# Performance work log

Measured on AMD Instinct MI355X. Metric: run time of the kernel, lower is better.

## Reference

```python
import jax, jax.numpy as jnp
import numpy as np

H, W, C_IN, C_OUT, N = 512, 512, 256, 256, 65536


def setup_inputs() -> dict:
    key = jax.random.key(0)
    k1, k2, k3, k4 = jax.random.split(key, 4)
    feature = jax.random.normal(k1, (1, C_IN, H, W), dtype=jnp.float32)
    weight = jax.random.normal(k2, (C_OUT, C_IN, 3, 3), dtype=jnp.float32) * 0.05
    # base sparse locations in the unpadded map; build 3x3 neighborhood indices
    # into the PADDED ([H+2, W+2]) map, exactly like F.pad + fancy indexing.
    base_h = jax.random.randint(k3, (N,), 0, H, dtype=jnp.int32)
    base_w = jax.random.randint(k4, (N,), 0, W, dtype=jnp.int32)
    dh = jnp.repeat(jnp.arange(3, dtype=jnp.int32), 3)  # [9]: 0,0,0,1,1,1,2,2,2
    dw = jnp.tile(jnp.arange(3, dtype=jnp.int32), 3)    # [9]: 0,1,2,0,1,2,...
    h_idx = base_h[None, :] + dh[:, None]  # [9, N], values in [0, H+1]
    w_idx = base_w[None, :] + dw[:, None]  # [9, N], values in [0, W+1]
    return {"feature": feature, "weight": weight, "h_idx": h_idx, "w_idx": w_idx}


def reference(feature, weight, h_idx, w_idx):
    # feature: [1, C, H, W]; weight: [Cout, C, 3, 3]; h_idx/w_idx: [9, N]
    C = feature.shape[1]
    out_ch = weight.shape[0]
    # F.pad(feature, [1,1,1,1])[0] -> [C, H+2, W+2]
    padded = jnp.pad(feature, ((0, 0), (0, 0), (1, 1), (1, 1)))[0]
    # gather 3x3 neighborhoods at sparse locations -> [C, 9, N]
    gathered = padded[:, h_idx, w_idx]
    # .view(9*C, -1): contiguous reshape gives row index c*9 + k
    g = gathered.reshape(C * 9, -1)  # [C*9, N]
    # kernel_d2s = weight.view(out, -1): row ordering c*9 + (kh*3+kw) matches
    k2d = weight.reshape(out_ch, -1)  # [Cout, C*9]
    return k2d @ g  # [Cout, N]
```

## Files before the change

### kernel.cpp

```cpp
#include <hip/hip_runtime.h>
#include <hip/hip_bf16.h>

#define HH 512
#define WW 512
#define CIN 256
#define COUT 256
#define NPTS 65536
#define PW 514
#define NPIX (PW * PW)
#define NKT 72

typedef __bf16 bf16x8 __attribute__((ext_vector_type(8)));
typedef float f32x16 __attribute__((ext_vector_type(16)));
typedef unsigned short us8 __attribute__((ext_vector_type(8)));

static __device__ __forceinline__ unsigned short f2bf(float f) {
  unsigned u = __builtin_bit_cast(unsigned, f);
  unsigned r = u + 0x7fffu + ((u >> 16) & 1u);
  return (unsigned short)(r >> 16);
}

static __device__ __forceinline__ void gload16(const void* g, void* l) {
  __builtin_amdgcn_global_load_lds(
      (const __attribute__((address_space(1))) unsigned int*)g,
      (__attribute__((address_space(3))) unsigned int*)l, 16, 0, 0);
}

__global__ __launch_bounds__(256) void prep_weight(const float* __restrict__ w,
                                                   unsigned short* __restrict__ A) {
  int i = blockIdx.x * 256 + threadIdx.x;
  int kt = i >> 13;
  int o  = i & 8191;
  int r  = o >> 5;
  int cp = (o >> 3) & 3;
  int j  = o & 7;
  int c  = cp ^ ((r >> 1) & 3);
  int k  = kt * 32 + c * 8 + j;
  int t  = k >> 8;
  int ci = k & 255;
  A[i] = f2bf(__builtin_nontemporal_load(&w[r * 2304 + ci * 9 + t]));
}

__global__ __launch_bounds__(256) void border_zero(unsigned short* __restrict__ Ft) {
  int g = blockIdx.x * 256 + threadIdx.x;
  if (g >= 2052 * 32) return;
  int p = g >> 5, c = g & 31;
  int py, px;
  if (p < 514)        { py = 0;        px = p; }
  else if (p < 1028)  { py = 513;      px = p - 514; }
  else if (p < 1540)  { py = p - 1027; px = 0; }
  else                { py = p - 1539; px = 513; }
  *(us8*)&Ft[((size_t)py * PW + px) * 256 + c * 8] = (us8){0, 0, 0, 0, 0, 0, 0, 0};
}

__global__ __launch_bounds__(256) void transpose_feat(const float* __restrict__ f,
                                                      unsigned short* __restrict__ Ft) {
  __shared__ unsigned short lds[64 * 264];
  int pix0 = blockIdx.x * 64;
  int y = pix0 >> 9, x0 = pix0 & 511;
  int tid = threadIdx.x;
  int p = tid & 63;
  int cb = tid >> 6;
  const float* src = f + pix0 + p;
  for (int c8 = 0; c8 < 8; ++c8) {
    us8 v;
#pragma unroll
    for (int j = 0; j < 8; ++j) {
      int ci = cb * 64 + c8 * 8 + j;
      v[j] = f2bf(__builtin_nontemporal_load(&src[ci * 262144]));
    }
    *(us8*)&lds[p * 264 + cb * 64 + c8 * 8] = v;
  }
  __syncthreads();
  int cic = tid & 31;
  int pr = tid >> 5;
  for (int g = 0; g < 8; ++g) {
    int p2 = pr + g * 8;
    us8 v = *(const us8*)&lds[p2 * 264 + cic * 8];
    *(us8*)&Ft[((size_t)((y + 1) * PW + x0 + 1 + p2)) * 256 + cic * 8] = v;
  }
}

__global__ __launch_bounds__(512, 2) void gemm_gather(
    const unsigned short* __restrict__ A,
    const unsigned short* __restrict__ Ft,
    const int* __restrict__ hidx,
    const int* __restrict__ widx,
    float* __restrict__ out) {
  __shared__ unsigned short lds[73728];
  unsigned short* ldsB = lds + 24576;

  int tid = threadIdx.x;
  int lane = tid & 63, wv = tid >> 6;
  int wm = wv & 1, wn = wv >> 1;
  int n0 = blockIdx.x << 8;

  int pxc = tid >> 3;
  int lcB = (tid & 7) ^ (pxc & 7);
  const unsigned short *FtP0, *FtP1, *FtP2, *FtP3;
  {
    FtP0 = Ft + (long)(hidx[n0 + pxc] * PW + widx[n0 + pxc]) * 256 + lcB * 8;
    FtP1 = Ft + (long)(hidx[n0 + 64 + pxc] * PW + widx[n0 + 64 + pxc]) * 256 + lcB * 8;
    FtP2 = Ft + (long)(hidx[n0 + 128 + pxc] * PW + widx[n0 + 128 + pxc]) * 256 + lcB * 8;
    FtP3 = Ft + (long)(hidx[n0 + 192 + pxc] * PW + widx[n0 + 192 + pxc]) * 256 + lcB * 8;
  }

#define STAGE_A(t_, ab_)                                                      \
  do {                                                                        \
    const unsigned short* g_ = A + (size_t)(t_) * 8192 + tid * 8;             \
    unsigned short* l_ = lds + (ab_) * 8192 + tid * 8;                        \
    gload16(g_, l_);                                                          \
    gload16(g_ + 4096, l_ + 4096);                                            \
  } while (0)

#define STAGE_BP(q_, bb_)                                                     \
  do {                                                                        \
    int tap_ = (q_) >> 2;                                                     \
    long off_ = (long)((tap_ / 3) * PW + (tap_ - (tap_ / 3) * 3)) * 256 +     \
                ((q_) & 3) * 64;                                              \
    unsigned short* l_ = ldsB + (bb_) * 16384 + tid * 8;                      \
    gload16(FtP0 + off_, l_);                                                 \
    gload16(FtP1 + off_, l_ + 4096);                                          \
    gload16(FtP2 + off_, l_ + 8192);                                          \
    gload16(FtP3 + off_, l_ + 12288);                                         \
  } while (0)

#define LDA(dst, ab_, kg_, mt_)                                               \
  do {                                                                        \
    int r_ = wm * 128 + (mt_) * 32 + (lane & 31);                             \
    int c_ = ((kg_) * 2 + (lane >> 5)) ^ ((r_ >> 1) & 3);                     \
    dst = *(const bf16x8*)&lds[(ab_) * 8192 + r_ * 32 + c_ * 8];              \
  } while (0)

#define LDB(dst, bb_, s_, kg_, nt_)                                           \
  do {                                                                        \
    int col_ = wn * 64 + (nt_) * 32 + (lane & 31);                            \
    int ph_ = ((s_) * 4 + (kg_) * 2 + (lane >> 5)) ^ (col_ & 7);              \
    dst = *(const bf16x8*)&ldsB[(bb_) * 16384 + col_ * 64 + ph_ * 8];         \
  } while (0)

#define MFMA8(a0, a1, a2, a3, b0, b1)                                         \
  do {                                                                        \
    __builtin_amdgcn_s_setprio(1);                                            \
    acc[0][0] = __builtin_amdgcn_mfma_f32_32x32x16_bf16(a0, b0, acc[0][0], 0, 0, 0); \
    acc[0][1] = __builtin_amdgcn_mfma_f32_32x32x16_bf16(a0, b1, acc[0][1], 0, 0, 0); \
    acc[1][0] = __builtin_amdgcn_mfma_f32_32x32x16_bf16(a1, b0, acc[1][0], 0, 0, 0); \
    acc[1][1] = __builtin_amdgcn_mfma_f32_32x32x16_bf16(a1, b1, acc[1][1], 0, 0, 0); \
    acc[2][0] = __builtin_amdgcn_mfma_f32_32x32x16_bf16(a2, b0, acc[2][0], 0, 0, 0); \
    acc[2][1] = __builtin_amdgcn_mfma_f32_32x32x16_bf16(a2, b1, acc[2][1], 0, 0, 0); \
    acc[3][0] = __builtin_amdgcn_mfma_f32_32x32x16_bf16(a3, b0, acc[3][0], 0, 0, 0); \
    acc[3][1] = __builtin_amdgcn_mfma_f32_32x32x16_bf16(a3, b1, acc[3][1], 0, 0, 0); \
    __builtin_amdgcn_s_setprio(0);                                            \
  } while (0)

#define HEAD()                                                                \
  do {                                                                        \
    asm volatile("s_waitcnt lgkmcnt(0)" ::: "memory");                        \
    asm volatile("s_waitcnt vmcnt(6)" ::: "memory");                          \
    __builtin_amdgcn_s_barrier();                                             \
    __builtin_amdgcn_sched_barrier(0);                                        \
  } while (0)

#define TILE(ab_, bb_, s_, ...)                                               \
  do {                                                                        \
    HEAD();                                                                   \
    bf16x8 xa0, xa1, xa2, xa3, xb0, xb1, ya0, ya1, ya2, ya3, yb0, yb1;        \
    LDA(xa0, ab_, 0, 0); LDA(xa1, ab_, 0, 1); LDA(xa2, ab_, 0, 2);            \
    LDA(xa3, ab_, 0, 3); LDB(xb0, bb_, s_, 0, 0); LDB(xb1, bb_, s_, 0, 1);    \
    __VA_ARGS__;                                                              \
    LDA(ya0, ab_, 1, 0); LDA(ya1, ab_, 1, 1); LDA(ya2, ab_, 1, 2);            \
    LDA(ya3, ab_, 1, 3); LDB(yb0, bb_, s_, 1, 0); LDB(yb1, bb_, s_, 1, 1);    \
    MFMA8(xa0, xa1, xa2, xa3, xb0, xb1);                                      \
    MFMA8(ya0, ya1, ya2, ya3, yb0, yb1);                                      \
  } while (0)

  f32x16 acc[4][2];
#pragma unroll
  for (int mt = 0; mt < 4; ++mt)
#pragma unroll
    for (int nt = 0; nt < 2; ++nt)
      acc[mt][nt] = (f32x16)(0.f);

  STAGE_BP(0, 0);
  STAGE_A(0, 0);
  STAGE_A(1, 1);
  STAGE_BP(1, 1);

  for (int P3 = 0; P3 < 12; ++P3) {
#pragma unroll
    for (int v = 0; v < 3; ++v) {
      int q = P3 * 3 + v;
      int t = 2 * q;
      TILE((2 * v) % 3, v, 0,
           STAGE_A((t + 2 < NKT ? t + 2 : NKT - 1), (2 * v + 2) % 3);
           STAGE_BP((q + 2 < 36 ? q + 2 : 35), (v + 2) % 3));
      TILE((2 * v + 1) % 3, v, 1,
           STAGE_A((t + 3 < NKT ? t + 3 : NKT - 1), (2 * v) % 3));
    }
  }

#undef STAGE_A
#undef STAGE_BP
#undef LDA
#undef LDB
#undef MFMA8
#undef HEAD
#undef TILE

  int colb = n0 + wn * 64 + (lane & 31);
  int rb = wm * 128 + ((lane >> 5) << 2);
#pragma unroll
  for (int mt = 0; mt < 4; ++mt)
#pragma unroll
    for (int nt = 0; nt < 2; ++nt)
#pragma unroll
      for (int r = 0; r < 16; ++r) {
        int row = rb + mt * 32 + (r & 3) + ((r >> 2) << 3);
        __builtin_nontemporal_store(acc[mt][nt][r],
                                    &out[(size_t)row * NPTS + colb + nt * 32]);
      }
}

__global__ __launch_bounds__(256) void naive_conv(const float* __restrict__ f,
                                                  const float* __restrict__ w,
                                                  const int* __restrict__ hi,
                                                  const int* __restrict__ wi,
                                                  float* __restrict__ out) {
  int idx = blockIdx.x * 256 + threadIdx.x;
  int n = idx & (NPTS - 1);
  int co = idx >> 16;
  int bh = hi[n] - 1;
  int bw = wi[n] - 1;
  float acc = 0.f;
  for (int ci = 0; ci < CIN; ++ci) {
    const float* fc = f + (size_t)ci * 262144;
    const float* wc = w + (size_t)co * 2304 + ci * 9;
#pragma unroll
    for (int t = 0; t < 9; ++t) {
      int y = bh + t / 3, x = bw + t % 3;
      float v = (y >= 0 && y < 512 && x >= 0 && x < 512) ? fc[y * 512 + x] : 0.f;
      acc += wc[t] * v;
    }
  }
  out[(size_t)co * NPTS + n] = acc;
}

extern "C" void kernel_launch(void* const* d_in, const int* in_sizes, int n_in,
                              void* d_out, int out_size, void* d_ws, size_t ws_size,
                              hipStream_t stream) {
  const float* feature = (const float*)d_in[0];
  const float* weight  = (const float*)d_in[1];
  const int* hidx      = (const int*)d_in[2];
  const int* widx      = (const int*)d_in[3];
  float* out           = (float*)d_out;

  const size_t FT_OFF = 2ull * 1024 * 1024;
  const size_t FT_BYTES = (size_t)NPIX * 256 * 2;
  const size_t NEED = FT_OFF + FT_BYTES;

  if (ws_size >= NEED) {
    unsigned short* Abf = (unsigned short*)d_ws;
    unsigned short* Ft = (unsigned short*)((char*)d_ws + FT_OFF);
    prep_weight<<<(NKT * 8192) / 256, 256, 0, stream>>>(weight, Abf);
    border_zero<<<(2052 * 32 + 255) / 256, 256, 0, stream>>>(Ft);
    transpose_feat<<<262144 / 64, 256, 0, stream>>>(feature, Ft);
    gemm_gather<<<NPTS / 256, 512, 0, stream>>>(Abf, Ft, hidx, widx, out);
  } else {
    naive_conv<<<(COUT * NPTS) / 256, 256, 0, stream>>>(feature, weight, hidx, widx, out);
  }
}
```

Measured before the change: 159.8 us.

## Split each K-tile into two barrier-separated MFMA phases interleaving LDS reads with staging

Restructures the inner tile so each k-tile runs in two halves, each with its own LDS fragment loads, a barrier plus lgkmcnt wait, and eight MFMAs over half the M-tiles. Global-to-LDS staging for A and B is split between the two halves, and the vmcnt wait and barrier move to the end of the tile, with an extra wait before the loop. The aim is a ping-pong style schedule where waves overlap LDS reads and async loads with MFMA work at lower register pressure. The cost is more barriers per tile and reloading A fragments in the second phase.

```diff
diff --git a/kernel.cpp b/kernel.cpp
--- a/kernel.cpp
+++ b/kernel.cpp
@@ -120,7 +120,7 @@
                 ((q_) & 3) * 64;                                              \
     unsigned short* l_ = ldsB + (bb_) * 16384 + tid * 8;                      \
     gload16(FtP0 + off_, l_);                                                 \
-    gload16(FtP1 + off_, l_ + 4096);                                          \
+    gload16(FtP1 + off_, l_ + 4096);                                         \
     gload16(FtP2 + off_, l_ + 8192);                                          \
     gload16(FtP3 + off_, l_ + 12288);                                         \
   } while (0)
@@ -139,39 +139,43 @@
     dst = *(const bf16x8*)&ldsB[(bb_) * 16384 + col_ * 64 + ph_ * 8];         \
   } while (0)
 
-#define MFMA8(a0, a1, a2, a3, b0, b1)                                         \
-  do {                                                                        \
+#define MF(x_, y_, z_) __builtin_amdgcn_mfma_f32_32x32x16_bf16(x_, y_, z_, 0, 0, 0)
+
+#define SYNC_LGKM()                                                           \
+  do {                                                                        \
+    __builtin_amdgcn_s_barrier();                                             \
+    asm volatile("s_waitcnt lgkmcnt(0)" ::: "memory");                        \
+    __builtin_amdgcn_sched_barrier(0);                                        \
+  } while (0)
+
+#define TILE(ab_, bb_, s_, STGA, STGB)                                        \
+  do {                                                                        \
+    bf16x8 a0, a1, a2, a3, b0, b1, b2, b3;                                    \
+    LDA(a0, ab_, 0, 0); LDA(a1, ab_, 0, 1);                                   \
+    LDA(a2, ab_, 1, 0); LDA(a3, ab_, 1, 1);                                   \
+    LDB(b0, bb_, s_, 0, 0); LDB(b1, bb_, s_, 0, 1);                           \
+    LDB(b2, bb_, s_, 1, 0); LDB(b3, bb_, s_, 1, 1);                           \
+    STGA;                                                                     \
+    SYNC_LGKM();                                                              \
     __builtin_amdgcn_s_setprio(1);                                            \
-    acc[0][0] = __builtin_amdgcn_mfma_f32_32x32x16_bf16(a0, b0, acc[0][0], 0, 0, 0); \
-    acc[0][1] = __builtin_amdgcn_mfma_f32_32x32x16_bf16(a0, b1, acc[0][1], 0, 0, 0); \
-    acc[1][0] = __builtin_amdgcn_mfma_f32_32x32x16_bf16(a1, b0, acc[1][0], 0, 0, 0); \
-    acc[1][1] = __builtin_amdgcn_mfma_f32_32x32x16_bf16(a1, b1, acc[1][1], 0, 0, 0); \
-    acc[2][0] = __builtin_amdgcn_mfma_f32_32x32x16_bf16(a2, b0, acc[2][0], 0, 0, 0); \
-    acc[2][1] = __builtin_amdgcn_mfma_f32_32x32x16_bf16(a2, b1, acc[2][1], 0, 0, 0); \
-    acc[3][0] = __builtin_amdgcn_mfma_f32_32x32x16_bf16(a3, b0, acc[3][0], 0, 0, 0); \
-    acc[3][1] = __builtin_amdgcn_mfma_f32_32x32x16_bf16(a3, b1, acc[3][1], 0, 0, 0); \
+    acc[0][0] = MF(a0, b0, acc[0][0]); acc[0][1] = MF(a0, b1, acc[0][1]);     \
+    acc[1][0] = MF(a1, b0, acc[1][0]); acc[1][1] = MF(a1, b1, acc[1][1]);     \
+    acc[0][0] = MF(a2, b2, acc[0][0]); acc[0][1] = MF(a2, b3, acc[0][1]);     \
+    acc[1][0] = MF(a3, b2, acc[1][0]); acc[1][1] = MF(a3, b3, acc[1][1]);     \
     __builtin_amdgcn_s_setprio(0);                                            \
-  } while (0)
-
-#define HEAD()                                                                \
-  do {                                                                        \
-    asm volatile("s_waitcnt lgkmcnt(0)" ::: "memory");                        \
+    __builtin_amdgcn_s_barrier();                                             \
+    LDA(a0, ab_, 0, 2); LDA(a1, ab_, 0, 3);                                   \
+    LDA(a2, ab_, 1, 2); LDA(a3, ab_, 1, 3);                                   \
+    STGB;                                                                     \
+    SYNC_LGKM();                                                              \
+    __builtin_amdgcn_s_setprio(1);                                            \
+    acc[2][0] = MF(a0, b0, acc[2][0]); acc[2][1] = MF(a0, b1, acc[2][1]);     \
+    acc[3][0] = MF(a1, b0, acc[3][0]); acc[3][1] = MF(a1, b1, acc[3][1]);     \
+    acc[2][0] = MF(a2, b2, acc[2][0]); acc[2][1] = MF(a2, b3, acc[2][1]);     \
+    acc[3][0] = MF(a3, b2, acc[3][0]); acc[3][1] = MF(a3, b3, acc[3][1]);     \
+    __builtin_amdgcn_s_setprio(0);                                            \
     asm volatile("s_waitcnt vmcnt(6)" ::: "memory");                          \
     __builtin_amdgcn_s_barrier();                                             \
-    __builtin_amdgcn_sched_barrier(0);                                        \
-  } while (0)
-
-#define TILE(ab_, bb_, s_, ...)                                               \
-  do {                                                                        \
-    HEAD();                                                                   \
-    bf16x8 xa0, xa1, xa2, xa3, xb0, xb1, ya0, ya1, ya2, ya3, yb0, yb1;        \
-    LDA(xa0, ab_, 0, 0); LDA(xa1, ab_, 0, 1); LDA(xa2, ab_, 0, 2);            \
-    LDA(xa3, ab_, 0, 3); LDB(xb0, bb_, s_, 0, 0); LDB(xb1, bb_, s_, 0, 1);    \
-    __VA_ARGS__;                                                              \
-    LDA(ya0, ab_, 1, 0); LDA(ya1, ab_, 1, 1); LDA(ya2, ab_, 1, 2);            \
-    LDA(ya3, ab_, 1, 3); LDB(yb0, bb_, s_, 1, 0); LDB(yb1, bb_, s_, 1, 1);    \
-    MFMA8(xa0, xa1, xa2, xa3, xb0, xb1);                                      \
-    MFMA8(ya0, ya1, ya2, ya3, yb0, yb1);                                      \
   } while (0)
 
   f32x16 acc[4][2];
@@ -185,6 +189,8 @@
   STAGE_A(0, 0);
   STAGE_A(1, 1);
   STAGE_BP(1, 1);
+  asm volatile("s_waitcnt vmcnt(6)" ::: "memory");
+  __builtin_amdgcn_s_barrier();
 
   for (int P3 = 0; P3 < 12; ++P3) {
 #pragma unroll
@@ -192,10 +198,11 @@
       int q = P3 * 3 + v;
       int t = 2 * q;
       TILE((2 * v) % 3, v, 0,
-           STAGE_A((t + 2 < NKT ? t + 2 : NKT - 1), (2 * v + 2) % 3);
+           STAGE_A((t + 2 < NKT ? t + 2 : NKT - 1), (2 * v + 2) % 3),
            STAGE_BP((q + 2 < 36 ? q + 2 : 35), (v + 2) % 3));
       TILE((2 * v + 1) % 3, v, 1,
-           STAGE_A((t + 3 < NKT ? t + 3 : NKT - 1), (2 * v) % 3));
+           STAGE_A((t + 3 < NKT ? t + 3 : NKT - 1), (2 * v) % 3),
+           (void)0);
     }
   }
 
@@ -203,8 +210,8 @@
 #undef STAGE_BP
 #undef LDA
 #undef LDB
-#undef MFMA8
-#undef HEAD
+#undef MF
+#undef SYNC_LGKM
 #undef TILE
 
   int colb = n0 + wn * 64 + (lane & 31);
```

New measurement: 161.2 us. About the same (+0.9%).

## Load weight fragments directly into registers and deepen B LDS pipeline

Applied to the files above, without the earlier changes.

Weights are pre-arranged by prep_weight into a layout that matches the MFMA fragments, so each wave reads its A operands straight from global memory (L2) into registers, double-buffered in aE/aO. This removes A staging through LDS and the A LDS reads. The freed LDS now holds a 4-deep ring for the gathered B tiles, and the main loop is simplified to one barrier per iteration. The trade-offs are that each wave re-fetches A from L2, which multiplies that traffic, register pressure goes up, and the loop relies on compiler-inserted vmcnt waits to order the async B loads into LDS.

```diff
diff --git a/kernel.cpp b/kernel.cpp
--- a/kernel.cpp
+++ b/kernel.cpp
@@ -27,18 +27,19 @@
 }
 
 __global__ __launch_bounds__(256) void prep_weight(const float* __restrict__ w,
-                                                   unsigned short* __restrict__ A) {
+                                                   unsigned short* __restrict__ A2) {
   int i = blockIdx.x * 256 + threadIdx.x;
   int kt = i >> 13;
-  int o  = i & 8191;
-  int r  = o >> 5;
-  int cp = (o >> 3) & 3;
-  int j  = o & 7;
-  int c  = cp ^ ((r >> 1) & 3);
-  int k  = kt * 32 + c * 8 + j;
+  int r2 = i & 8191;
+  int fr = r2 >> 9;
+  int l  = (r2 >> 3) & 63;
+  int j  = i & 7;
+  int wm = fr >> 3, mt = (fr >> 1) & 3, kg = fr & 1;
+  int row = wm * 128 + mt * 32 + (l & 31);
+  int k  = kt * 32 + kg * 16 + (l >> 5) * 8 + j;
   int t  = k >> 8;
   int ci = k & 255;
-  A[i] = f2bf(__builtin_nontemporal_load(&w[r * 2304 + ci * 9 + t]));
+  A2[i] = f2bf(__builtin_nontemporal_load(&w[row * 2304 + ci * 9 + t]));
 }
 
 __global__ __launch_bounds__(256) void border_zero(unsigned short* __restrict__ Ft) {
@@ -82,13 +83,12 @@
 }
 
 __global__ __launch_bounds__(512, 2) void gemm_gather(
-    const unsigned short* __restrict__ A,
+    const unsigned short* __restrict__ A2,
     const unsigned short* __restrict__ Ft,
     const int* __restrict__ hidx,
     const int* __restrict__ widx,
     float* __restrict__ out) {
-  __shared__ unsigned short lds[73728];
-  unsigned short* ldsB = lds + 24576;
+  __shared__ unsigned short lds[65536];
 
   int tid = threadIdx.x;
   int lane = tid & 63, wv = tid >> 6;
@@ -105,73 +105,47 @@
     FtP3 = Ft + (long)(hidx[n0 + 192 + pxc] * PW + widx[n0 + 192 + pxc]) * 256 + lcB * 8;
   }
 
-#define STAGE_A(t_, ab_)                                                      \
-  do {                                                                        \
-    const unsigned short* g_ = A + (size_t)(t_) * 8192 + tid * 8;             \
-    unsigned short* l_ = lds + (ab_) * 8192 + tid * 8;                        \
-    gload16(g_, l_);                                                          \
-    gload16(g_ + 4096, l_ + 4096);                                            \
-  } while (0)
-
 #define STAGE_BP(q_, bb_)                                                     \
   do {                                                                        \
     int tap_ = (q_) >> 2;                                                     \
     long off_ = (long)((tap_ / 3) * PW + (tap_ - (tap_ / 3) * 3)) * 256 +     \
                 ((q_) & 3) * 64;                                              \
-    unsigned short* l_ = ldsB + (bb_) * 16384 + tid * 8;                      \
+    unsigned short* l_ = lds + (bb_) * 16384 + tid * 8;                       \
     gload16(FtP0 + off_, l_);                                                 \
     gload16(FtP1 + off_, l_ + 4096);                                          \
     gload16(FtP2 + off_, l_ + 8192);                                          \
     gload16(FtP3 + off_, l_ + 12288);                                         \
   } while (0)
 
-#define LDA(dst, ab_, kg_, mt_)                                               \
-  do {                                                                        \
-    int r_ = wm * 128 + (mt_) * 32 + (lane & 31);                             \
-    int c_ = ((kg_) * 2 + (lane >> 5)) ^ ((r_ >> 1) & 3);                     \
-    dst = *(const bf16x8*)&lds[(ab_) * 8192 + r_ * 32 + c_ * 8];              \
-  } while (0)
-
-#define LDB(dst, bb_, s_, kg_, nt_)                                           \
-  do {                                                                        \
-    int col_ = wn * 64 + (nt_) * 32 + (lane & 31);                            \
-    int ph_ = ((s_) * 4 + (kg_) * 2 + (lane >> 5)) ^ (col_ & 7);              \
-    dst = *(const bf16x8*)&ldsB[(bb_) * 16384 + col_ * 64 + ph_ * 8];         \
-  } while (0)
-
-#define MFMA8(a0, a1, a2, a3, b0, b1)                                         \
+#define LOADA(dst_, kt_)                                                      \
+  do {                                                                        \
+    const unsigned short* ga_ = A2 + (size_t)(kt_) * 8192 + wm * 4096 + lane * 8; \
+    _Pragma("unroll") for (int f_ = 0; f_ < 8; ++f_)                          \
+        dst_[f_] = *(const bf16x8*)&ga_[f_ * 512];                            \
+  } while (0)
+
+#define LDB4(dst_, bb_, s_)                                                   \
+  do {                                                                        \
+    _Pragma("unroll") for (int kg_ = 0; kg_ < 2; ++kg_)                       \
+        _Pragma("unroll") for (int nt_ = 0; nt_ < 2; ++nt_) {                 \
+      int col_ = wn * 64 + nt_ * 32 + (lane & 31);                            \
+      int ph_ = ((s_) * 4 + kg_ * 2 + (lane >> 5)) ^ (col_ & 7);              \
+      dst_[kg_ * 2 + nt_] =                                                   \
+          *(const bf16x8*)&lds[(bb_) * 16384 + col_ * 64 + ph_ * 8];          \
+    }                                                                         \
+  } while (0)
+
+#define MF(x_, y_, z_) __builtin_amdgcn_mfma_f32_32x32x16_bf16(x_, y_, z_, 0, 0, 0)
+
+#define MFMA16(a_, b_)                                                        \
   do {                                                                        \
     __builtin_amdgcn_s_setprio(1);                                            \
-    acc[0][0] = __builtin_amdgcn_mfma_f32_32x32x16_bf16(a0, b0, acc[0][0], 0, 0, 0); \
-    acc[0][1] = __builtin_amdgcn_mfma_f32_32x32x16_bf16(a0, b1, acc[0][1], 0, 0, 0); \
-    acc[1][0] = __builtin_amdgcn_mfma_f32_32x32x16_bf16(a1, b0, acc[1][0], 0, 0, 0); \
-    acc[1][1] = __builtin_amdgcn_mfma_f32_32x32x16_bf16(a1, b1, acc[1][1], 0, 0, 0); \
-    acc[2][0] = __builtin_amdgcn_mfma_f32_32x32x16_bf16(a2, b0, acc[2][0], 0, 0, 0); \
-    acc[2][1] = __builtin_amdgcn_mfma_f32_32x32x16_bf16(a2, b1, acc[2][1], 0, 0, 0); \
-    acc[3][0] = __builtin_amdgcn_mfma_f32_32x32x16_bf16(a3, b0, acc[3][0], 0, 0, 0); \
-    acc[3][1] = __builtin_amdgcn_mfma_f32_32x32x16_bf16(a3, b1, acc[3][1], 0, 0, 0); \
+    _Pragma("unroll") for (int mt_ = 0; mt_ < 4; ++mt_)                       \
+        _Pragma("unroll") for (int kg_ = 0; kg_ < 2; ++kg_)                   \
+            _Pragma("unroll") for (int nt_ = 0; nt_ < 2; ++nt_)               \
+                acc[mt_][nt_] =                                               \
+                    MF(a_[mt_ * 2 + kg_], b_[kg_ * 2 + nt_], acc[mt_][nt_]);  \
     __builtin_amdgcn_s_setprio(0);                                            \
-  } while (0)
-
-#define HEAD()                                                                \
-  do {                                                                        \
-    asm volatile("s_waitcnt lgkmcnt(0)" ::: "memory");                        \
-    asm volatile("s_waitcnt vmcnt(6)" ::: "memory");                          \
-    __builtin_amdgcn_s_barrier();                                             \
-    __builtin_amdgcn_sched_barrier(0);                                        \
-  } while (0)
-
-#define TILE(ab_, bb_, s_, ...)                                               \
-  do {                                                                        \
-    HEAD();                                                                   \
-    bf16x8 xa0, xa1, xa2, xa3, xb0, xb1, ya0, ya1, ya2, ya3, yb0, yb1;        \
-    LDA(xa0, ab_, 0, 0); LDA(xa1, ab_, 0, 1); LDA(xa2, ab_, 0, 2);            \
-    LDA(xa3, ab_, 0, 3); LDB(xb0, bb_, s_, 0, 0); LDB(xb1, bb_, s_, 0, 1);    \
-    __VA_ARGS__;                                                              \
-    LDA(ya0, ab_, 1, 0); LDA(ya1, ab_, 1, 1); LDA(ya2, ab_, 1, 2);            \
-    LDA(ya3, ab_, 1, 3); LDB(yb0, bb_, s_, 1, 0); LDB(yb1, bb_, s_, 1, 1);    \
-    MFMA8(xa0, xa1, xa2, xa3, xb0, xb1);                                      \
-    MFMA8(ya0, ya1, ya2, ya3, yb0, yb1);                                      \
   } while (0)
 
   f32x16 acc[4][2];
@@ -181,31 +155,34 @@
     for (int nt = 0; nt < 2; ++nt)
       acc[mt][nt] = (f32x16)(0.f);
 
+  bf16x8 aE[8], aO[8], bX[4], bY[4];
+
+  LOADA(aE, 0);
   STAGE_BP(0, 0);
-  STAGE_A(0, 0);
-  STAGE_A(1, 1);
   STAGE_BP(1, 1);
-
-  for (int P3 = 0; P3 < 12; ++P3) {
-#pragma unroll
-    for (int v = 0; v < 3; ++v) {
-      int q = P3 * 3 + v;
-      int t = 2 * q;
-      TILE((2 * v) % 3, v, 0,
-           STAGE_A((t + 2 < NKT ? t + 2 : NKT - 1), (2 * v + 2) % 3);
-           STAGE_BP((q + 2 < 36 ? q + 2 : 35), (v + 2) % 3));
-      TILE((2 * v + 1) % 3, v, 1,
-           STAGE_A((t + 3 < NKT ? t + 3 : NKT - 1), (2 * v) % 3));
-    }
-  }
-
-#undef STAGE_A
+  asm volatile("s_waitcnt vmcnt(4)" ::: "memory");
+  __builtin_amdgcn_s_barrier();
+  __builtin_amdgcn_sched_barrier(0);
+
+  for (int p = 0; p < 36; ++p) {
+    int t = 2 * p;
+    LOADA(aO, (t + 1 < NKT ? t + 1 : NKT - 1));
+    LDB4(bX, p & 3, 0);
+    if (p + 2 < 36) STAGE_BP(p + 2, (p + 2) & 3);
+    MFMA16(aE, bX);
+    LOADA(aE, (t + 2 < NKT ? t + 2 : NKT - 1));
+    LDB4(bY, p & 3, 1);
+    MFMA16(aO, bY);
+    asm volatile("s_waitcnt lgkmcnt(0)" ::: "memory");
+    __builtin_amdgcn_s_barrier();
+    __builtin_amdgcn_sched_barrier(0);
+  }
+
 #undef STAGE_BP
-#undef LDA
-#undef LDB
-#undef MFMA8
-#undef HEAD
-#undef TILE
+#undef LOADA
+#undef LDB4
+#undef MF
+#undef MFMA16
 
   int colb = n0 + wn * 64 + (lane & 31);
   int rb = wm * 128 + ((lane >> 5) << 2);
```

Measured after the change: 165.6 us. 1.04x slower.
